# Optimization experiments

Hardware: AMD Instinct MI355X
Metric: run time of the kernel (lower is better)

## Reference

```python
import jax, jax.numpy as jnp
import numpy as np

B = 65536
H = 1024          # hidden_dimension
D_OUT = 2         # output_dimension
N_EXPERTS = 10


def setup_inputs() -> dict:
    key = jax.random.key(0)
    ks = jax.random.split(key, 9)
    s = 0.02
    return {
        "x": jax.random.normal(ks[0], (B, 12), dtype=jnp.float32),
        "W1": jax.random.normal(ks[1], (H, 1), dtype=jnp.float32) * s,    # fc1 weight [out,in]
        "b1": jax.random.normal(ks[2], (H,), dtype=jnp.float32) * s,
        "Wmeta": jax.random.normal(ks[3], (N_EXPERTS, H), dtype=jnp.float32) * s,  # row i = fc_meta[i].weight[:,0]
        "bmeta": jax.random.normal(ks[4], (N_EXPERTS, H), dtype=jnp.float32) * s,  # row i = fc_meta[i].bias
        "W2": jax.random.normal(ks[5], (H, H), dtype=jnp.float32) * s,
        "b2": jax.random.normal(ks[6], (H,), dtype=jnp.float32) * s,
        "W3": jax.random.normal(ks[7], (D_OUT, H), dtype=jnp.float32) * s,
        "b3": jax.random.normal(ks[8], (D_OUT,), dtype=jnp.float32) * s,
    }


def reference(x, W1, b1, Wmeta, bmeta, W2, b2, W3, b3):
    one_hot = x[:, 0:10]          # [B, 10] expert selection weights
    delta = x[:, 10:11]           # [B, 1]
    phi = x[:, 11:12]             # [B, 1]
    # fc1(delta): [B,1] @ [1,H]
    x1 = delta * W1[:, 0] + b1    # [B, H]
    # expert i output: phi * Wmeta[i] + bmeta[i]; one-hot weighted sum over experts
    # sum_i one_hot[:,i]*(phi*Wmeta[i]+bmeta[i]) = phi*(one_hot@Wmeta) + one_hot@bmeta
    x2 = phi * (one_hot @ Wmeta) + one_hot @ bmeta  # [B, H]
    h = jax.nn.relu(x1 + x2)
    h = jax.nn.relu(h @ W2.T + b2)                  # fc2 + relu
    return h @ W3.T + b3                            # fc3 -> [B, 2]
```

## Files before the change

### kernel.cpp

```cpp
#include <hip/hip_runtime.h>
#include <stdint.h>

#define NROWS 65536
#define HD 1024

typedef __attribute__((ext_vector_type(8))) short bf16x8;
typedef __attribute__((ext_vector_type(16))) float f32x16;

typedef __attribute__((address_space(1))) const unsigned int* gas_ptr;
typedef __attribute__((address_space(3))) unsigned int* las_ptr;

__device__ __forceinline__ unsigned short f2bf(float f) {
  union { float f; uint32_t u; } v; v.f = f;
  uint32_t u = v.u;
  return (unsigned short)((u + 0x7fffu + ((u >> 16) & 1u)) >> 16);
}

__device__ __forceinline__ void gl16(const void* g, void* l) {
  __builtin_amdgcn_global_load_lds((gas_ptr)g, (las_ptr)l, 16, 0, 0);
}

__global__ void k_w2bf(const float* __restrict__ W2, unsigned short* __restrict__ W2bf) {
  int i = blockIdx.x * 256 + threadIdx.x;
  int c = i >> 7, g = i & 127;
  const float4* s4 = (const float4*)(W2 + (size_t)c * HD + g * 8);
  float4 a = s4[0], b = s4[1];
  uint4 pk;
  pk.x = (uint32_t)f2bf(a.x) | ((uint32_t)f2bf(a.y) << 16);
  pk.y = (uint32_t)f2bf(a.z) | ((uint32_t)f2bf(a.w) << 16);
  pk.z = (uint32_t)f2bf(b.x) | ((uint32_t)f2bf(b.y) << 16);
  pk.w = (uint32_t)f2bf(b.z) | ((uint32_t)f2bf(b.w) << 16);
  int gs = g ^ (c & 7);
  *(uint4*)(W2bf + (size_t)c * HD + gs * 8) = pk;
}

__global__ __launch_bounds__(512) void k_layer1(
    const float* __restrict__ x, const float* __restrict__ W1,
    const float* __restrict__ b1, const float* __restrict__ Wmeta,
    const float* __restrict__ bmeta, unsigned short* __restrict__ h) {
  __shared__ float xs[128 * 12];
  int r0 = blockIdx.x * 128;
  int t = threadIdx.x;
  int j0 = t * 2;
  float w1a = W1[j0], w1b = W1[j0 + 1];
  float b1a = b1[j0], b1b = b1[j0 + 1];
  float wma[10], wmb[10], bma[10], bmb[10];
#pragma unroll
  for (int e = 0; e < 10; e++) {
    float2 wmv = *(const float2*)(Wmeta + e * HD + j0);
    float2 bmv = *(const float2*)(bmeta + e * HD + j0);
    wma[e] = wmv.x; wmb[e] = wmv.y; bma[e] = bmv.x; bmb[e] = bmv.y;
  }
  for (int i = t; i < 128 * 12; i += 512) xs[i] = x[(size_t)r0 * 12 + i];
  __syncthreads();
  for (int r = 0; r < 128; r++) {
    const float* xr = xs + r * 12;
    float delta = xr[10], phi = xr[11];
    float s1a = 0.f, s1b = 0.f, s2a = 0.f, s2b = 0.f;
#pragma unroll
    for (int e = 0; e < 10; e++) {
      float oh = xr[e];
      s1a = fmaf(oh, wma[e], s1a);
      s1b = fmaf(oh, wmb[e], s1b);
      s2a = fmaf(oh, bma[e], s2a);
      s2b = fmaf(oh, bmb[e], s2b);
    }
    float pa = fmaf(delta, w1a, b1a) + fmaf(phi, s1a, s2a);
    float pb = fmaf(delta, w1b, b1b) + fmaf(phi, s1b, s2b);
    pa = fmaxf(pa, 0.f); pb = fmaxf(pb, 0.f);
    uint32_t pk = (uint32_t)f2bf(pa) | ((uint32_t)f2bf(pb) << 16);
    int rr = r0 + r;
    int gs = (j0 >> 3) ^ (rr & 7);
    *(uint32_t*)(h + (size_t)rr * HD + gs * 8 + (j0 & 7)) = pk;
  }
}

__global__ __launch_bounds__(512, 2) void k_gemm(
    const unsigned short* __restrict__ h, const unsigned short* __restrict__ W2bf,
    const float* __restrict__ b2, const float* __restrict__ W3,
    float* __restrict__ partial) {
  extern __shared__ char lds[];
  int tid = threadIdx.x;
  int bx = blockIdx.x;
  int rt = bx >> 2, ct = bx & 3;
  size_t r0 = (size_t)rt * 256;
  int c0 = ct * 256;
  int w = tid >> 6, lane = tid & 63;
  int wm = w >> 2, wn = w & 3;
  int l31 = lane & 31, hi = lane >> 5;

  f32x16 acc[4][2];
#pragma unroll
  for (int rb = 0; rb < 4; rb++)
#pragma unroll
    for (int cb = 0; cb < 2; cb++)
#pragma unroll
      for (int i = 0; i < 16; i++) acc[rb][cb][i] = 0.f;

  auto stage = [&](int buf, int t) {
    size_t k0 = (size_t)t * 64;
    char* lA = lds + buf * 65536;
    char* lB = lA + 32768;
#pragma unroll
    for (int q = 0; q < 4; q++) {
      int s = tid + 512 * q;
      int row = s >> 3, g8 = (s & 7) * 8;
      gl16(h + ((size_t)(r0 + row)) * HD + k0 + g8, lA + (size_t)s * 16);
      gl16(W2bf + ((size_t)(c0 + row)) * HD + k0 + g8, lB + (size_t)s * 16);
    }
  };

  stage(0, 0);
  __syncthreads();
  int cur = 0;
  for (int t = 0; t < 16; t++) {
    if (t + 1 < 16) stage(cur ^ 1, t + 1);
    const char* lA = lds + cur * 65536;
    const char* lB = lA + 32768;
#pragma unroll
    for (int kk = 0; kk < 4; kk++) {
      int gc = kk * 2 + hi;
      bf16x8 av[4], bv[2];
#pragma unroll
      for (int rb = 0; rb < 4; rb++) {
        int row = wm * 128 + rb * 32 + l31;
        av[rb] = *(const bf16x8*)(lA + row * 128 + ((gc ^ (row & 7)) << 4));
      }
#pragma unroll
      for (int cb = 0; cb < 2; cb++) {
        int crow = wn * 64 + cb * 32 + l31;
        bv[cb] = *(const bf16x8*)(lB + crow * 128 + ((gc ^ (crow & 7)) << 4));
      }
#pragma unroll
      for (int rb = 0; rb < 4; rb++)
#pragma unroll
        for (int cb = 0; cb < 2; cb++)
          acc[rb][cb] = __builtin_amdgcn_mfma_f32_32x32x16_bf16(av[rb], bv[cb], acc[rb][cb], 0, 0, 0);
    }
    __syncthreads();
    cur ^= 1;
  }

  float b2c[2], w30[2], w31[2];
#pragma unroll
  for (int cb = 0; cb < 2; cb++) {
    int c = c0 + wn * 64 + cb * 32 + l31;
    b2c[cb] = b2[c];
    w30[cb] = W3[c];
    w31[cb] = W3[HD + c];
  }
  float* sOutW = (float*)lds;
#pragma unroll
  for (int rb = 0; rb < 4; rb++) {
#pragma unroll
    for (int reg = 0; reg < 16; reg++) {
      float v0 = fmaxf(acc[rb][0][reg] + b2c[0], 0.f);
      float v1 = fmaxf(acc[rb][1][reg] + b2c[1], 0.f);
      float o0 = v0 * w30[0] + v1 * w30[1];
      float o1 = v0 * w31[0] + v1 * w31[1];
#pragma unroll
      for (int m = 16; m >= 1; m >>= 1) {
        o0 += __shfl_xor(o0, m);
        o1 += __shfl_xor(o1, m);
      }
      if (l31 == 0) {
        int rowf = (reg & 3) + 8 * (reg >> 2) + 4 * hi;
        int row = wm * 128 + rb * 32 + rowf;
        sOutW[(wn * 256 + row) * 2 + 0] = o0;
        sOutW[(wn * 256 + row) * 2 + 1] = o1;
      }
    }
  }
  __syncthreads();
  {
    int i = tid;
    float s = sOutW[i] + sOutW[512 + i] + sOutW[1024 + i] + sOutW[1536 + i];
    partial[(size_t)ct * (NROWS * 2) + r0 * 2 + i] = s;
  }
}

__global__ void k_reduce(const float* __restrict__ partial, const float* __restrict__ b3,
                         float* __restrict__ out) {
  int i = blockIdx.x * 256 + threadIdx.x;
  float s = b3[i & 1] + partial[i] + partial[131072 + i] + partial[262144 + i] + partial[393216 + i];
  out[i] = s;
}

extern "C" void kernel_launch(void* const* d_in, const int* in_sizes, int n_in,
                              void* d_out, int out_size, void* d_ws, size_t ws_size,
                              hipStream_t stream) {
  const float* x     = (const float*)d_in[0];
  const float* W1    = (const float*)d_in[1];
  const float* b1    = (const float*)d_in[2];
  const float* Wmeta = (const float*)d_in[3];
  const float* bmeta = (const float*)d_in[4];
  const float* W2    = (const float*)d_in[5];
  const float* b2    = (const float*)d_in[6];
  const float* W3    = (const float*)d_in[7];
  const float* b3    = (const float*)d_in[8];
  float* out = (float*)d_out;

  char* ws = (char*)d_ws;
  unsigned short* hbuf  = (unsigned short*)ws;
  unsigned short* W2bf  = (unsigned short*)(ws + (size_t)NROWS * HD * 2);
  float* partial = (float*)(ws + (size_t)NROWS * HD * 2 + (size_t)HD * HD * 2);

  hipFuncSetAttribute((const void*)k_gemm, hipFuncAttributeMaxDynamicSharedMemorySize, 131072);

  k_w2bf<<<512, 256, 0, stream>>>(W2, W2bf);
  k_layer1<<<512, 512, 0, stream>>>(x, W1, b1, Wmeta, bmeta, hbuf);
  k_gemm<<<1024, 512, 131072, stream>>>(hbuf, W2bf, b2, W3, partial);
  k_reduce<<<512, 256, 0, stream>>>(partial, b3, out);
}
```

Before: 240.6 us.

## Deepen GEMM K-pipeline to 4-slot ring with interleaved loads and barriers

Restructures the bf16 GEMM main loop from double-buffered 64-wide K tiles into a 4-slot ring of 32-wide K tiles, prefetching three tiles ahead. Each half-tile issues its global-to-LDS loads between the LDS reads and the MFMA block. It waits with explicit vmcnt/lgkmcnt counters and raises wave priority around the MFMAs. The LDS swizzle changes to match the 64-byte rows, which also changes how layer1 and the W2 conversion write their swizzled data. The aim is to hide global load latency and keep MFMAs busy, at the cost of more barriers per K step and fragile hand-tuned wait counts.

```diff
diff --git a/kernel.cpp b/kernel.cpp
--- a/kernel.cpp
+++ b/kernel.cpp
@@ -3,6 +3,7 @@
 
 #define NROWS 65536
 #define HD 1024
+#define KTILES 32
 
 typedef __attribute__((ext_vector_type(8))) short bf16x8;
 typedef __attribute__((ext_vector_type(16))) float f32x16;
@@ -30,7 +31,7 @@
   pk.y = (uint32_t)f2bf(a.z) | ((uint32_t)f2bf(a.w) << 16);
   pk.z = (uint32_t)f2bf(b.x) | ((uint32_t)f2bf(b.y) << 16);
   pk.w = (uint32_t)f2bf(b.z) | ((uint32_t)f2bf(b.w) << 16);
-  int gs = g ^ (c & 7);
+  int gs = (g & 124) | ((g & 3) ^ ((c >> 1) & 3));
   *(uint4*)(W2bf + (size_t)c * HD + gs * 8) = pk;
 }
 
@@ -53,6 +54,7 @@
   }
   for (int i = t; i < 128 * 12; i += 512) xs[i] = x[(size_t)r0 * 12 + i];
   __syncthreads();
+  int g = j0 >> 3;
   for (int r = 0; r < 128; r++) {
     const float* xr = xs + r * 12;
     float delta = xr[10], phi = xr[11];
@@ -70,7 +72,7 @@
     pa = fmaxf(pa, 0.f); pb = fmaxf(pb, 0.f);
     uint32_t pk = (uint32_t)f2bf(pa) | ((uint32_t)f2bf(pb) << 16);
     int rr = r0 + r;
-    int gs = (j0 >> 3) ^ (rr & 7);
+    int gs = (g & 124) | ((g & 3) ^ ((rr >> 1) & 3));
     *(uint32_t*)(h + (size_t)rr * HD + gs * 8 + (j0 & 7)) = pk;
   }
 }
@@ -97,48 +99,54 @@
 #pragma unroll
       for (int i = 0; i < 16; i++) acc[rb][cb][i] = 0.f;
 
-  auto stage = [&](int buf, int t) {
-    size_t k0 = (size_t)t * 64;
-    char* lA = lds + buf * 65536;
-    char* lB = lA + 32768;
-#pragma unroll
-    for (int q = 0; q < 4; q++) {
-      int s = tid + 512 * q;
-      int row = s >> 3, g8 = (s & 7) * 8;
-      gl16(h + ((size_t)(r0 + row)) * HD + k0 + g8, lA + (size_t)s * 16);
-      gl16(W2bf + ((size_t)(c0 + row)) * HD + k0 + g8, lB + (size_t)s * 16);
-    }
+  auto stage1 = [&](int T, int q) {
+    int slot = T & 3;
+    char* base = lds + (size_t)slot * 32768;
+    int s = tid + 512 * q;
+    int row = s >> 2, off8 = (s & 3) * 8;
+    gl16(h    + (r0 + row) * (size_t)HD + T * 32 + off8, base + (size_t)s * 16);
+    gl16(W2bf + (size_t)(c0 + row) * HD + T * 32 + off8, base + 16384 + (size_t)s * 16);
   };
 
-  stage(0, 0);
-  __syncthreads();
-  int cur = 0;
-  for (int t = 0; t < 16; t++) {
-    if (t + 1 < 16) stage(cur ^ 1, t + 1);
-    const char* lA = lds + cur * 65536;
-    const char* lB = lA + 32768;
-#pragma unroll
-    for (int kk = 0; kk < 4; kk++) {
-      int gc = kk * 2 + hi;
+  stage1(0, 0); stage1(0, 1);
+  stage1(1, 0); stage1(1, 1);
+  stage1(2, 0); stage1(2, 1);
+  asm volatile("s_waitcnt vmcnt(8)" ::: "memory");
+  __builtin_amdgcn_s_barrier();
+
+  for (int T = 0; T < KTILES; T++) {
+    const char* lA = lds + (size_t)(T & 3) * 32768;
+    const char* lB = lA + 16384;
+#pragma unroll
+    for (int p = 0; p < 2; p++) {
+      int g = p * 2 + hi;
       bf16x8 av[4], bv[2];
 #pragma unroll
       for (int rb = 0; rb < 4; rb++) {
         int row = wm * 128 + rb * 32 + l31;
-        av[rb] = *(const bf16x8*)(lA + row * 128 + ((gc ^ (row & 7)) << 4));
+        av[rb] = *(const bf16x8*)(lA + row * 64 + ((g ^ ((row >> 1) & 3)) << 4));
       }
 #pragma unroll
       for (int cb = 0; cb < 2; cb++) {
         int crow = wn * 64 + cb * 32 + l31;
-        bv[cb] = *(const bf16x8*)(lB + crow * 128 + ((gc ^ (crow & 7)) << 4));
-      }
+        bv[cb] = *(const bf16x8*)(lB + crow * 64 + ((g ^ ((crow >> 1) & 3)) << 4));
+      }
+      if (T < KTILES - 3) stage1(T + 3, p);
+      if (p == 1) asm volatile("s_waitcnt vmcnt(8)" ::: "memory");
+      asm volatile("" ::: "memory");
+      __builtin_amdgcn_s_barrier();
+      asm volatile("s_waitcnt lgkmcnt(0)" ::: "memory");
+      __builtin_amdgcn_sched_barrier(0);
+      __builtin_amdgcn_s_setprio(1);
 #pragma unroll
       for (int rb = 0; rb < 4; rb++)
 #pragma unroll
         for (int cb = 0; cb < 2; cb++)
           acc[rb][cb] = __builtin_amdgcn_mfma_f32_32x32x16_bf16(av[rb], bv[cb], acc[rb][cb], 0, 0, 0);
+      __builtin_amdgcn_s_setprio(0);
+      asm volatile("" ::: "memory");
+      __builtin_amdgcn_s_barrier();
     }
-    __syncthreads();
-    cur ^= 1;
   }
 
   float b2c[2], w30[2], w31[2];
```

Measured after the change: 254.6 us. +5.8%, slower.

## Shrink GEMM tiles to 128x128 with single-buffered LDS and more blocks per CU

Applied to the files above, without the earlier changes.

The fc2 GEMM changes from 256x256 tiles with a 128KB double-buffered LDS ring and 512 threads to 128x128 tiles, 256 threads and about 34KB of static LDS, launched as 4096 blocks with a blockIdx swizzle that groups column tiles together. The LDS layout and the XOR swizzle used by the bf16 producers are rewritten to suit 64-byte half-tiles. The fc3 epilogue now does its cross-lane reduction through padded LDS instead of shuffles, and k_reduce sums 8 partials instead of 4. The aim is higher occupancy and better wave scheduling to hide latency. In exchange it loses the double-buffer overlap, reuses each loaded byte over fewer FLOPs, and writes twice as much partial data.

```diff
diff --git a/kernel.cpp b/kernel.cpp
--- a/kernel.cpp
+++ b/kernel.cpp
@@ -30,7 +30,7 @@
   pk.y = (uint32_t)f2bf(a.z) | ((uint32_t)f2bf(a.w) << 16);
   pk.z = (uint32_t)f2bf(b.x) | ((uint32_t)f2bf(b.y) << 16);
   pk.w = (uint32_t)f2bf(b.z) | ((uint32_t)f2bf(b.w) << 16);
-  int gs = g ^ (c & 7);
+  int gs = (g & 124) | ((g & 3) ^ ((c >> 1) & 3));
   *(uint4*)(W2bf + (size_t)c * HD + gs * 8) = pk;
 }
 
@@ -53,6 +53,7 @@
   }
   for (int i = t; i < 128 * 12; i += 512) xs[i] = x[(size_t)r0 * 12 + i];
   __syncthreads();
+  int g = j0 >> 3;
   for (int r = 0; r < 128; r++) {
     const float* xr = xs + r * 12;
     float delta = xr[10], phi = xr[11];
@@ -70,75 +71,71 @@
     pa = fmaxf(pa, 0.f); pb = fmaxf(pb, 0.f);
     uint32_t pk = (uint32_t)f2bf(pa) | ((uint32_t)f2bf(pb) << 16);
     int rr = r0 + r;
-    int gs = (j0 >> 3) ^ (rr & 7);
+    int gs = (g & 124) | ((g & 3) ^ ((rr >> 1) & 3));
     *(uint32_t*)(h + (size_t)rr * HD + gs * 8 + (j0 & 7)) = pk;
   }
 }
 
-__global__ __launch_bounds__(512, 2) void k_gemm(
+__global__ __launch_bounds__(256, 3) void k_gemm(
     const unsigned short* __restrict__ h, const unsigned short* __restrict__ W2bf,
     const float* __restrict__ b2, const float* __restrict__ W3,
     float* __restrict__ partial) {
-  extern __shared__ char lds[];
+  __shared__ char lds[34816];
   int tid = threadIdx.x;
-  int bx = blockIdx.x;
-  int rt = bx >> 2, ct = bx & 3;
-  size_t r0 = (size_t)rt * 256;
-  int c0 = ct * 256;
+  int b = (int)blockIdx.x;
+  int bx = ((b & 7) << 9) | (b >> 3);
+  int rt = bx >> 3, ct = bx & 7;
+  size_t r0 = (size_t)rt * 128;
+  int c0 = ct * 128;
   int w = tid >> 6, lane = tid & 63;
-  int wm = w >> 2, wn = w & 3;
+  int wm = w >> 1, wn = w & 1;
   int l31 = lane & 31, hi = lane >> 5;
-
-  f32x16 acc[4][2];
-#pragma unroll
-  for (int rb = 0; rb < 4; rb++)
+  int sw = (l31 >> 1) & 3;
+
+  f32x16 acc[2][2];
+#pragma unroll
+  for (int rb = 0; rb < 2; rb++)
 #pragma unroll
     for (int cb = 0; cb < 2; cb++)
 #pragma unroll
       for (int i = 0; i < 16; i++) acc[rb][cb][i] = 0.f;
 
-  auto stage = [&](int buf, int t) {
-    size_t k0 = (size_t)t * 64;
-    char* lA = lds + buf * 65536;
-    char* lB = lA + 32768;
-#pragma unroll
-    for (int q = 0; q < 4; q++) {
-      int s = tid + 512 * q;
-      int row = s >> 3, g8 = (s & 7) * 8;
-      gl16(h + ((size_t)(r0 + row)) * HD + k0 + g8, lA + (size_t)s * 16);
-      gl16(W2bf + ((size_t)(c0 + row)) * HD + k0 + g8, lB + (size_t)s * 16);
-    }
-  };
-
-  stage(0, 0);
-  __syncthreads();
-  int cur = 0;
-  for (int t = 0; t < 16; t++) {
-    if (t + 1 < 16) stage(cur ^ 1, t + 1);
-    const char* lA = lds + cur * 65536;
-    const char* lB = lA + 32768;
-#pragma unroll
-    for (int kk = 0; kk < 4; kk++) {
-      int gc = kk * 2 + hi;
-      bf16x8 av[4], bv[2];
-#pragma unroll
-      for (int rb = 0; rb < 4; rb++) {
-        int row = wm * 128 + rb * 32 + l31;
-        av[rb] = *(const bf16x8*)(lA + row * 128 + ((gc ^ (row & 7)) << 4));
+  int arow0 = (wm * 64 + 0  + l31) * 64;
+  int arow1 = (wm * 64 + 32 + l31) * 64;
+  int brow0 = (wn * 64 + 0  + l31) * 64;
+  int brow1 = (wn * 64 + 32 + l31) * 64;
+
+  for (int T = 0; T < 16; T++) {
+#pragma unroll
+    for (int q = 0; q < 2; q++) {
+      int s = tid + 256 * q;
+      int row = s >> 2, g4 = s & 3;
+      const unsigned short* hsrc = h    + (r0 + row) * (size_t)HD + T * 64 + g4 * 8;
+      const unsigned short* wsrc = W2bf + (size_t)(c0 + row) * HD + T * 64 + g4 * 8;
+      gl16(hsrc,      lds +         (size_t)s * 16);
+      gl16(hsrc + 32, lds +  8192 + (size_t)s * 16);
+      gl16(wsrc,      lds + 16384 + (size_t)s * 16);
+      gl16(wsrc + 32, lds + 24576 + (size_t)s * 16);
+    }
+    __syncthreads();
+#pragma unroll
+    for (int p = 0; p < 2; p++) {
+      const char* lA = lds + p * 8192;
+      const char* lB = lds + 16384 + p * 8192;
+#pragma unroll
+      for (int kl = 0; kl < 2; kl++) {
+        int slot = ((kl * 2 + hi) ^ sw) << 4;
+        bf16x8 a0 = *(const bf16x8*)(lA + arow0 + slot);
+        bf16x8 a1 = *(const bf16x8*)(lA + arow1 + slot);
+        bf16x8 b0 = *(const bf16x8*)(lB + brow0 + slot);
+        bf16x8 b1 = *(const bf16x8*)(lB + brow1 + slot);
+        acc[0][0] = __builtin_amdgcn_mfma_f32_32x32x16_bf16(a0, b0, acc[0][0], 0, 0, 0);
+        acc[0][1] = __builtin_amdgcn_mfma_f32_32x32x16_bf16(a0, b1, acc[0][1], 0, 0, 0);
+        acc[1][0] = __builtin_amdgcn_mfma_f32_32x32x16_bf16(a1, b0, acc[1][0], 0, 0, 0);
+        acc[1][1] = __builtin_amdgcn_mfma_f32_32x32x16_bf16(a1, b1, acc[1][1], 0, 0, 0);
       }
-#pragma unroll
-      for (int cb = 0; cb < 2; cb++) {
-        int crow = wn * 64 + cb * 32 + l31;
-        bv[cb] = *(const bf16x8*)(lB + crow * 128 + ((gc ^ (crow & 7)) << 4));
-      }
-#pragma unroll
-      for (int rb = 0; rb < 4; rb++)
-#pragma unroll
-        for (int cb = 0; cb < 2; cb++)
-          acc[rb][cb] = __builtin_amdgcn_mfma_f32_32x32x16_bf16(av[rb], bv[cb], acc[rb][cb], 0, 0, 0);
-    }
-    __syncthreads();
-    cur ^= 1;
+    }
+    __syncthreads();
   }
 
   float b2c[2], w30[2], w31[2];
@@ -149,40 +146,43 @@
     w30[cb] = W3[c];
     w31[cb] = W3[HD + c];
   }
-  float* sOutW = (float*)lds;
-#pragma unroll
-  for (int rb = 0; rb < 4; rb++) {
+  float2* sE = (float2*)lds;
+#pragma unroll
+  for (int rb = 0; rb < 2; rb++) {
+    __syncthreads();
 #pragma unroll
     for (int reg = 0; reg < 16; reg++) {
       float v0 = fmaxf(acc[rb][0][reg] + b2c[0], 0.f);
       float v1 = fmaxf(acc[rb][1][reg] + b2c[1], 0.f);
-      float o0 = v0 * w30[0] + v1 * w30[1];
-      float o1 = v0 * w31[0] + v1 * w31[1];
-#pragma unroll
-      for (int m = 16; m >= 1; m >>= 1) {
-        o0 += __shfl_xor(o0, m);
-        o1 += __shfl_xor(o1, m);
-      }
-      if (l31 == 0) {
-        int rowf = (reg & 3) + 8 * (reg >> 2) + 4 * hi;
-        int row = wm * 128 + rb * 32 + rowf;
-        sOutW[(wn * 256 + row) * 2 + 0] = o0;
-        sOutW[(wn * 256 + row) * 2 + 1] = o1;
-      }
-    }
-  }
-  __syncthreads();
-  {
-    int i = tid;
-    float s = sOutW[i] + sOutW[512 + i] + sOutW[1024 + i] + sOutW[1536 + i];
-    partial[(size_t)ct * (NROWS * 2) + r0 * 2 + i] = s;
+      float2 o;
+      o.x = v0 * w30[0] + v1 * w30[1];
+      o.y = v0 * w31[0] + v1 * w31[1];
+      int rowf = (reg & 3) + 8 * (reg >> 2) + 4 * hi;
+      int line = (wm * 32 + rowf) * 2 + wn;
+      sE[line * 33 + l31] = o;
+    }
+    __syncthreads();
+    int half = tid & 1, tgt = tid >> 1;
+    int d = tgt & 1, rowf_t = (tgt >> 1) & 31, bi = tgt >> 6;
+    int line0 = (bi * 32 + rowf_t) * 2 + half;
+    const float* sf = (const float*)lds;
+    float s = 0.f;
+#pragma unroll
+    for (int j = 0; j < 32; j++) s += sf[(line0 * 33 + j) * 2 + d];
+    s += __shfl_xor(s, 1);
+    if (half == 0) {
+      int row = bi * 64 + rb * 32 + rowf_t;
+      partial[(size_t)ct * (NROWS * 2) + (r0 + row) * 2 + d] = s;
+    }
   }
 }
 
 __global__ void k_reduce(const float* __restrict__ partial, const float* __restrict__ b3,
                          float* __restrict__ out) {
   int i = blockIdx.x * 256 + threadIdx.x;
-  float s = b3[i & 1] + partial[i] + partial[131072 + i] + partial[262144 + i] + partial[393216 + i];
+  float s = b3[i & 1];
+#pragma unroll
+  for (int ctt = 0; ctt < 8; ctt++) s += partial[(size_t)ctt * 131072 + i];
   out[i] = s;
 }
 
@@ -205,10 +205,8 @@
   unsigned short* W2bf  = (unsigned short*)(ws + (size_t)NROWS * HD * 2);
   float* partial = (float*)(ws + (size_t)NROWS * HD * 2 + (size_t)HD * HD * 2);
 
-  hipFuncSetAttribute((const void*)k_gemm, hipFuncAttributeMaxDynamicSharedMemorySize, 131072);
-
   k_w2bf<<<512, 256, 0, stream>>>(W2, W2bf);
   k_layer1<<<512, 512, 0, stream>>>(x, W1, b1, Wmeta, bmeta, hbuf);
-  k_gemm<<<1024, 512, 131072, stream>>>(hbuf, W2bf, b2, W3, partial);
+  k_gemm<<<4096, 256, 0, stream>>>(hbuf, W2bf, b2, W3, partial);
   k_reduce<<<512, 256, 0, stream>>>(partial, b3, out);
 }
```

Result: faster. 208.7 us (-13.3%).
